# Kernel tuning notes

Measured on AMD Instinct MI355X. Metric: run time of the kernel, lower is better.

The kernel has to match this reference:

```python
import jax, jax.numpy as jnp
import numpy as np

NUM_CLASSES = 10
THRESHOLD = 2e-4
ENT_COEF = 2e-4
COS_EPS = 1e-8
LOG_EPS = 1e-12


def setup_inputs() -> dict:
    key = jax.random.key(0)
    k1, k2, k3 = jax.random.split(key, 3)
    B, C, H, W = 256, 256, 8, 8
    M, F = 2000, C * H * W
    z = jax.random.normal(k1, (B, C, H, W), dtype=jnp.float32)
    labels = jax.random.randint(k2, (B,), 0, NUM_CLASSES)
    # kaiming-uniform-like init for the memory table
    bound = float(np.sqrt(6.0 / F))
    memory = jax.random.uniform(k3, (M, F), dtype=jnp.float32, minval=-bound, maxval=bound)
    return {"z": z, "labels": labels, "memory": memory}


def _shrink_l1norm(w):
    # hardshrink (strict |x| > lambda) then L1 renormalize along memories
    w = jnp.where(jnp.abs(w) > THRESHOLD, w, jnp.zeros_like(w))
    return w / jnp.sum(jnp.abs(w), axis=1, keepdims=True)


def _entropy_loss(w):
    return ENT_COEF * jnp.sum(-w * jnp.log(w + LOG_EPS))


def reference(z, labels, memory):
    B, C, H, W = z.shape
    M, F = memory.shape
    zf = z.reshape(B, F)
    # cosine similarity without materializing (B, M, F): dot / max(||z||*||m||, eps)
    nz = jnp.linalg.norm(zf, axis=1)              # (B,)
    nm = jnp.linalg.norm(memory, axis=1)          # (M,)
    logit = (zf @ memory.T) / jnp.maximum(nz[:, None] * nm[None, :], COS_EPS)  # (B, M)
    mem_weight = jax.nn.softmax(logit, axis=1)
    # per-class masks: memory slots are partitioned contiguously per class
    mem_per_class = M // NUM_CLASSES
    cls_of_mem = jnp.arange(M) // mem_per_class   # (M,)
    m1 = (cls_of_mem[None, :] == labels[:, None]).astype(mem_weight.dtype)  # target mask
    m2 = 1.0 - m1
    w_t = _shrink_l1norm(mem_weight * m1)
    w_nt = _shrink_l1norm(mem_weight * m2)
    z_hat_target = (w_t @ memory).reshape(B, C, H, W)
    z_hat_non_target = (w_nt @ memory).reshape(B, C, H, W)
    return (z_hat_target, z_hat_non_target, _entropy_loss(w_t), _entropy_loss(w_nt))
```

## Files before the change

kernel.cpp:

```cpp
#include <hip/hip_runtime.h>
#include <math.h>

#define BATCH 256
#define FDIM 16384
#define MSLOTS 2000
#define MPAD 2048
#define NCLS 10
#define MPC 200
#define NFB (FDIM / 64)

static constexpr float THRESH = 2e-4f;
static constexpr float ENTC   = 2e-4f;
static constexpr float CEPS   = 1e-8f;
static constexpr float LEPS   = 1e-12f;

using bf16x8 = __attribute__((ext_vector_type(8))) short;
using f32x4  = __attribute__((ext_vector_type(4))) float;
using us8    = __attribute__((ext_vector_type(8))) unsigned short;

__device__ __forceinline__ unsigned short f2bf(float f) {
  unsigned u = __float_as_uint(f);
  unsigned r = u + 0x7fffu + ((u >> 16) & 1u);
  return (unsigned short)(r >> 16);
}
__device__ __forceinline__ float bf2f(unsigned short b) {
  return __uint_as_float(((unsigned)b) << 16);
}

__device__ __forceinline__ void gload_lds16(const unsigned short* g, unsigned short* l) {
  __builtin_amdgcn_global_load_lds(
      (const __attribute__((address_space(1))) void*)g,
      (__attribute__((address_space(3))) void*)l, 16, 0, 0);
}

__device__ __forceinline__ float waveReduceSum(float v) {
#pragma unroll
  for (int o = 32; o > 0; o >>= 1) v += __shfl_xor(v, o);
  return v;
}
__device__ __forceinline__ float waveReduceMax(float v) {
#pragma unroll
  for (int o = 32; o > 0; o >>= 1) v = fmaxf(v, __shfl_xor(v, o));
  return v;
}


__global__ __launch_bounds__(256) void convert_all_kernel(
    const float* __restrict__ z, const float* __restrict__ mem,
    unsigned short* __restrict__ zb, unsigned short* __restrict__ mb,
    unsigned short* __restrict__ mt, float* __restrict__ npart) {
  __shared__ unsigned int P[64 * 34];
  __shared__ float rsum[64][17];
  const int tid = threadIdx.x;
  const int f0 = blockIdx.x * 64;
  const int yt = blockIdx.y;
  const bool isMem = (yt < MPAD / 64);
  const int r0 = isMem ? yt * 64 : (yt - MPAD / 64) * 64;
  const float* src = isMem ? mem : z;
  unsigned short* dst = isMem ? mb : zb;

  const int q = tid & 15;
  const int mb0 = tid >> 4;

#pragma unroll
  for (int it = 0; it < 4; ++it) {
    const int m = mb0 + it * 16;
    const int gr = r0 + m;
    float4 v = make_float4(0.f, 0.f, 0.f, 0.f);
    if (!isMem || gr < MSLOTS)
      v = *reinterpret_cast<const float4*>(&src[(size_t)gr * FDIM + f0 + q * 4]);
    rsum[m][q] = fmaf(v.x, v.x, fmaf(v.y, v.y, fmaf(v.z, v.z, v.w * v.w)));
    unsigned lo = ((unsigned)f2bf(v.y) << 16) | f2bf(v.x);
    unsigned hi = ((unsigned)f2bf(v.w) << 16) | f2bf(v.z);
    *reinterpret_cast<uint2*>(&dst[(size_t)gr * FDIM + f0 + q * 4]) = make_uint2(lo, hi);
    if (isMem) {
      const int x = (m >> 1) & 15;
      const int col = 2 * (q ^ x);
      *reinterpret_cast<uint2*>(&P[m * 34 + col]) = make_uint2(lo, hi);
    }
  }
  __syncthreads();

  if (isMem) {
    const int h = tid & 7;
    const int j = tid >> 3;
    unsigned p[8];
#pragma unroll
    for (int s = 0; s < 8; ++s) {
      const int m = 8 * h + s;
      const int col = j ^ (((m >> 1) & 15) << 1);
      p[s] = P[m * 34 + col];
    }
    unsigned lo[4], hi[4];
#pragma unroll
    for (int t = 0; t < 4; ++t) {
      const unsigned p0 = p[2 * t], p1 = p[2 * t + 1];
      lo[t] = (p1 << 16) | (p0 & 0xFFFFu);
      hi[t] = (p1 & 0xFFFF0000u) | (p0 >> 16);
    }
    const size_t base0 = (size_t)(f0 + 2 * j) * MPAD + r0 + h * 8;
    *reinterpret_cast<uint4*>(&mt[base0])        = make_uint4(lo[0], lo[1], lo[2], lo[3]);
    *reinterpret_cast<uint4*>(&mt[base0 + MPAD]) = make_uint4(hi[0], hi[1], hi[2], hi[3]);
  }

  if (tid < 64) {
    float s = 0.f;
#pragma unroll
    for (int c = 0; c < 16; ++c) s += rsum[tid][c];
    const int row = isMem ? (r0 + tid) : (MPAD + r0 + tid);
    npart[(size_t)row * NFB + blockIdx.x] = s;
  }
}

__global__ __launch_bounds__(64) void normfin_kernel(const float* __restrict__ npart,
                                                     float* __restrict__ nm,
                                                     float* __restrict__ nz) {
  const int row = blockIdx.x;
  const int lane = threadIdx.x;
  const float* p = npart + (size_t)row * NFB;
  float s = 0.f;
#pragma unroll
  for (int k = 0; k < NFB / 64; ++k) s += p[lane + k * 64];
  s = waveReduceSum(s);
  if (lane == 0) {
    float v = sqrtf(s);
    if (row < MPAD) nm[row] = v;
    else            nz[row - MPAD] = v;
  }
}

#define G1_BM 128
#define G1_BN 64
#define G1_BK 64
#define SPLITK 8
#define KCHUNK (FDIM / SPLITK)

__global__ __launch_bounds__(256, 2) void gemm1_mfma(const unsigned short* __restrict__ zb,
                                                     const unsigned short* __restrict__ mb,
                                                     float* __restrict__ part) {
  __shared__ unsigned short As[G1_BM * G1_BK];
  __shared__ unsigned short Bs[G1_BN * G1_BK];
  const int tid = threadIdx.x;
  const int lane = tid & 63, wid = tid >> 6;
  const int bn0 = blockIdx.x * G1_BN;
  const int bm0 = blockIdx.y * G1_BM;
  const int kbase = blockIdx.z * KCHUNK;
  const int wr = wid >> 1, wc = wid & 1;
  const int l8 = lane >> 3, l7 = lane & 7;
  const int r16 = lane & 15, klane = lane >> 4;

  f32x4 acc[4][2] = {};

  for (int kt = 0; kt < KCHUNK; kt += G1_BK) {
    const int kg = kbase + kt;
#pragma unroll
    for (int it = 0; it < 4; ++it) {
      int c = wid + it * 4;
      int r = c * 8 + l8;
      int src = (l7 ^ (r & 7)) << 3;
      gload_lds16(&zb[(size_t)(bm0 + r) * FDIM + kg + src], &As[c * 512]);
    }
#pragma unroll
    for (int it = 0; it < 2; ++it) {
      int c = wid + it * 4;
      int r = c * 8 + l8;
      int src = (l7 ^ (r & 7)) << 3;
      gload_lds16(&mb[(size_t)(bn0 + r) * FDIM + kg + src], &Bs[c * 512]);
    }
    __syncthreads();
#pragma unroll
    for (int s = 0; s < 2; ++s) {
      bf16x8 a[4], bb[2];
#pragma unroll
      for (int i = 0; i < 4; ++i) {
        int r = wr * 64 + i * 16 + r16;
        int p = (s * 4 + klane) ^ (r & 7);
        a[i] = *reinterpret_cast<const bf16x8*>(&As[r * 64 + p * 8]);
      }
#pragma unroll
      for (int j = 0; j < 2; ++j) {
        int r = wc * 32 + j * 16 + r16;
        int p = (s * 4 + klane) ^ (r & 7);
        bb[j] = *reinterpret_cast<const bf16x8*>(&Bs[r * 64 + p * 8]);
      }
#pragma unroll
      for (int i = 0; i < 4; ++i)
#pragma unroll
        for (int j = 0; j < 2; ++j)
          acc[i][j] = __builtin_amdgcn_mfma_f32_16x16x32_bf16(a[i], bb[j], acc[i][j], 0, 0, 0);
    }
    __syncthreads();
  }
  const int rgrp = lane >> 4;
  float* pbase = part + (size_t)blockIdx.z * BATCH * MPAD;
#pragma unroll
  for (int i = 0; i < 4; ++i)
#pragma unroll
    for (int j = 0; j < 2; ++j)
#pragma unroll
      for (int rg = 0; rg < 4; ++rg) {
        int row = bm0 + wr * 64 + i * 16 + rgrp * 4 + rg;
        int col = bn0 + wc * 32 + j * 16 + r16;
        pbase[(size_t)row * MPAD + col] = acc[i][j][rg];
      }
}

__global__ __launch_bounds__(256) void softmax2_kernel(const float* __restrict__ part,
                                                       const float* __restrict__ nzv,
                                                       const float* __restrict__ nmv,
                                                       const int* __restrict__ labels,
                                                       unsigned short* __restrict__ wt,
                                                       unsigned short* __restrict__ wn,
                                                       float* __restrict__ ent) {
  const int b = blockIdx.x, tid = threadIdx.x;
  __shared__ float sh[MSLOTS];
  __shared__ float red[4], red2[4];
  const float nzb = nzv[b];
  float mx = -3.4e38f;
  for (int m = tid; m < MSLOTS; m += 256) {
    float s = 0.f;
#pragma unroll
    for (int sp = 0; sp < SPLITK; ++sp)
      s += part[((size_t)sp * BATCH + b) * MPAD + m];
    float v = s / fmaxf(nzb * nmv[m], CEPS);
    sh[m] = v; mx = fmaxf(mx, v);
  }
  mx = waveReduceMax(mx);
  if ((tid & 63) == 0) red[tid >> 6] = mx;
  __syncthreads();
  mx = fmaxf(fmaxf(red[0], red[1]), fmaxf(red[2], red[3]));
  __syncthreads();

  float s = 0.f;
  for (int m = tid; m < MSLOTS; m += 256) {
    float e = expf(sh[m] - mx); sh[m] = e; s += e;
  }
  s = waveReduceSum(s);
  if ((tid & 63) == 0) red[tid >> 6] = s;
  __syncthreads();
  s = red[0] + red[1] + red[2] + red[3];
  __syncthreads();

  const float inv = 1.f / s;
  const int c = labels[b];
  const int t0 = c * MPC, t1 = t0 + MPC;
  float st = 0.f, sn = 0.f;
  for (int m = tid; m < MSLOTS; m += 256) {
    float w = sh[m] * inv;
    float k = (w > THRESH) ? w : 0.f;
    sh[m] = k;
    bool tgt = (m >= t0) && (m < t1);
    st += tgt ? k : 0.f;
    sn += tgt ? 0.f : k;
  }
  st = waveReduceSum(st); sn = waveReduceSum(sn);
  if ((tid & 63) == 0) { red[tid >> 6] = st; red2[tid >> 6] = sn; }
  __syncthreads();
  st = red[0] + red[1] + red[2] + red[3];
  sn = red2[0] + red2[1] + red2[2] + red2[3];
  __syncthreads();

  const float rt = 1.f / st, rn = 1.f / sn;
  float et = 0.f, en = 0.f;
  unsigned short* wtr = wt + (size_t)b * MPAD;
  unsigned short* wnr = wn + (size_t)b * MPAD;
  for (int m = tid; m < MPAD; m += 256) {
    float a = 0.f, cn = 0.f;
    if (m < MSLOTS) {
      float k = sh[m];
      bool tgt = (m >= t0) && (m < t1);
      a  = tgt ? k * rt : 0.f;
      cn = tgt ? 0.f : k * rn;
      et -= a  * logf(a  + LEPS);
      en -= cn * logf(cn + LEPS);
    }
    wtr[m] = f2bf(a);
    wnr[m] = f2bf(cn);
  }
  et = waveReduceSum(et); en = waveReduceSum(en);
  if ((tid & 63) == 0) { red[tid >> 6] = et; red2[tid >> 6] = en; }
  __syncthreads();
  if (tid == 0) {
    ent[b]         = red[0] + red[1] + red[2] + red[3];
    ent[BATCH + b] = red2[0] + red2[1] + red2[2] + red2[3];
  }
}

#define G2_BM 128
#define G2_BN 128
#define G2_BK 64

__global__ __launch_bounds__(512, 2) void gemm23_mfma(const unsigned short* __restrict__ wt,
                                                      const unsigned short* __restrict__ wn,
                                                      const unsigned short* __restrict__ mt,
                                                      float* __restrict__ out) {
  __shared__ unsigned short At[G2_BM * G2_BK];
  __shared__ unsigned short An[G2_BM * G2_BK];
  __shared__ unsigned short Bs[G2_BN * G2_BK];
  const int tid = threadIdx.x, lane = tid & 63, wid = tid >> 6;
  const int bn0 = blockIdx.x * G2_BN;
  const int bm0 = blockIdx.y * G2_BM;
  const int wr = wid >> 2, wc = wid & 3;
  const int l8 = lane >> 3, l7 = lane & 7;
  const int r16 = lane & 15, klane = lane >> 4;

  f32x4 acct[4][2] = {}, accn[4][2] = {};

  for (int k0 = 0; k0 < MPAD; k0 += G2_BK) {
#pragma unroll
    for (int it = 0; it < 2; ++it) {
      int c = wid + it * 8;
      int r = c * 8 + l8;
      int src = (l7 ^ (r & 7)) << 3;
      gload_lds16(&wt[(size_t)(bm0 + r) * MPAD + k0 + src], &At[c * 512]);
      gload_lds16(&wn[(size_t)(bm0 + r) * MPAD + k0 + src], &An[c * 512]);
      gload_lds16(&mt[(size_t)(bn0 + r) * MPAD + k0 + src], &Bs[c * 512]);
    }
    __syncthreads();
#pragma unroll
    for (int s = 0; s < 2; ++s) {
      bf16x8 at[4], an[4], bb[2];
#pragma unroll
      for (int i = 0; i < 4; ++i) {
        int r = wr * 64 + i * 16 + r16;
        int p = (s * 4 + klane) ^ (r & 7);
        at[i] = *reinterpret_cast<const bf16x8*>(&At[r * 64 + p * 8]);
        an[i] = *reinterpret_cast<const bf16x8*>(&An[r * 64 + p * 8]);
      }
#pragma unroll
      for (int j = 0; j < 2; ++j) {
        int r = wc * 32 + j * 16 + r16;
        int p = (s * 4 + klane) ^ (r & 7);
        bb[j] = *reinterpret_cast<const bf16x8*>(&Bs[r * 64 + p * 8]);
      }
#pragma unroll
      for (int i = 0; i < 4; ++i)
#pragma unroll
        for (int j = 0; j < 2; ++j) {
          acct[i][j] = __builtin_amdgcn_mfma_f32_16x16x32_bf16(at[i], bb[j], acct[i][j], 0, 0, 0);
          accn[i][j] = __builtin_amdgcn_mfma_f32_16x16x32_bf16(an[i], bb[j], accn[i][j], 0, 0, 0);
        }
    }
    __syncthreads();
  }
  float* outn = out + (size_t)BATCH * FDIM;
  const int rgrp = lane >> 4;
#pragma unroll
  for (int i = 0; i < 4; ++i)
#pragma unroll
    for (int j = 0; j < 2; ++j)
#pragma unroll
      for (int rg = 0; rg < 4; ++rg) {
        size_t off = (size_t)(bm0 + wr * 64 + i * 16 + rgrp * 4 + rg) * FDIM
                   + bn0 + wc * 32 + j * 16 + r16;
        out[off]  = acct[i][j][rg];
        outn[off] = accn[i][j][rg];
      }
}

__global__ __launch_bounds__(256) void entreduce_kernel(const float* __restrict__ ent,
                                                        float* __restrict__ out) {
  const int tid = threadIdx.x;
  float v = ent[tid];
  float u = ent[BATCH + tid];
  v = waveReduceSum(v); u = waveReduceSum(u);
  __shared__ float r1[4], r2[4];
  if ((tid & 63) == 0) { r1[tid >> 6] = v; r2[tid >> 6] = u; }
  __syncthreads();
  if (tid == 0) {
    out[(size_t)2 * BATCH * FDIM]     = ENTC * (r1[0] + r1[1] + r1[2] + r1[3]);
    out[(size_t)2 * BATCH * FDIM + 1] = ENTC * (r2[0] + r2[1] + r2[2] + r2[3]);
  }
}

#define NM_OFF    0
#define NZ_OFF    2048
#define LOGIT_OFF 4096
#define WT_OFF    (LOGIT_OFF + 512000)
#define WNT_OFF   (WT_OFF + 512000)
#define ENT_OFF   (WNT_OFF + 512000)

__global__ __launch_bounds__(256) void rownorm_kernel(const float* __restrict__ x,
                                                      float* __restrict__ out, int cols) {
  const int r = blockIdx.x;
  const float4* xr = reinterpret_cast<const float4*>(x) + (size_t)r * (cols >> 2);
  const int n4 = cols >> 2;
  float s = 0.f;
  for (int i = threadIdx.x; i < n4; i += 256) {
    float4 v = xr[i];
    s = fmaf(v.x, v.x, s); s = fmaf(v.y, v.y, s);
    s = fmaf(v.z, v.z, s); s = fmaf(v.w, v.w, s);
  }
  s = waveReduceSum(s);
  __shared__ float red[4];
  if ((threadIdx.x & 63) == 0) red[threadIdx.x >> 6] = s;
  __syncthreads();
  if (threadIdx.x == 0) out[r] = sqrtf(red[0] + red[1] + red[2] + red[3]);
}

#define O1_BM 64
#define O1_BN 32
#define O1_BK 64
__global__ __launch_bounds__(256) void gemm1_kernel(const float* __restrict__ z,
                                                    const float* __restrict__ mem,
                                                    const float* __restrict__ nzv,
                                                    const float* __restrict__ nmv,
                                                    float* __restrict__ logit) {
  __shared__ float As[O1_BK][O1_BM];
  __shared__ float Bs[O1_BK][O1_BN];
  const int tid = threadIdx.x;
  const int bm0 = blockIdx.y * O1_BM;
  const int bn0 = blockIdx.x * O1_BN;
  const int tm = tid >> 4, tn = tid & 15;
  float acc[4][2] = {};
  for (int k0 = 0; k0 < FDIM; k0 += O1_BK) {
#pragma unroll
    for (int it = 0; it < 4; ++it) {
      int i = tid + it * 256;
      int row = i >> 4, c4 = i & 15;
      float4 v = *reinterpret_cast<const float4*>(&z[(size_t)(bm0 + row) * FDIM + k0 + c4 * 4]);
      As[c4 * 4 + 0][row] = v.x; As[c4 * 4 + 1][row] = v.y;
      As[c4 * 4 + 2][row] = v.z; As[c4 * 4 + 3][row] = v.w;
    }
#pragma unroll
    for (int it = 0; it < 2; ++it) {
      int i = tid + it * 256;
      int row = i >> 4, c4 = i & 15;
      int gm = bn0 + row;
      float4 v = make_float4(0.f, 0.f, 0.f, 0.f);
      if (gm < MSLOTS)
        v = *reinterpret_cast<const float4*>(&mem[(size_t)gm * FDIM + k0 + c4 * 4]);
      Bs[c4 * 4 + 0][row] = v.x; Bs[c4 * 4 + 1][row] = v.y;
      Bs[c4 * 4 + 2][row] = v.z; Bs[c4 * 4 + 3][row] = v.w;
    }
    __syncthreads();
#pragma unroll
    for (int kk = 0; kk < O1_BK; ++kk) {
      const float* ap = &As[kk][tm * 4];
      const float* bp = &Bs[kk][tn * 2];
      float a0 = ap[0], a1 = ap[1], a2 = ap[2], a3 = ap[3];
      float b0 = bp[0], b1 = bp[1];
      acc[0][0] = fmaf(a0, b0, acc[0][0]); acc[0][1] = fmaf(a0, b1, acc[0][1]);
      acc[1][0] = fmaf(a1, b0, acc[1][0]); acc[1][1] = fmaf(a1, b1, acc[1][1]);
      acc[2][0] = fmaf(a2, b0, acc[2][0]); acc[2][1] = fmaf(a2, b1, acc[2][1]);
      acc[3][0] = fmaf(a3, b0, acc[3][0]); acc[3][1] = fmaf(a3, b1, acc[3][1]);
    }
    __syncthreads();
  }
  float nzr[4];
#pragma unroll
  for (int i = 0; i < 4; ++i) nzr[i] = nzv[bm0 + tm * 4 + i];
#pragma unroll
  for (int j = 0; j < 2; ++j) {
    int col = bn0 + tn * 2 + j;
    if (col < MSLOTS) {
      float nmr = nmv[col];
#pragma unroll
      for (int i = 0; i < 4; ++i)
        logit[(size_t)(bm0 + tm * 4 + i) * MSLOTS + col] = acc[i][j] / fmaxf(nzr[i] * nmr, CEPS);
    }
  }
}

__global__ __launch_bounds__(256) void softmax_kernel(const float* __restrict__ logit,
                                                      const int* __restrict__ labels,
                                                      float* __restrict__ wt,
                                                      float* __restrict__ wnt,
                                                      float* __restrict__ ent) {
  const int b = blockIdx.x;
  const int tid = threadIdx.x;
  __shared__ float sh[MSLOTS];
  __shared__ float red[4], red2[4];
  const float* lrow = logit + (size_t)b * MSLOTS;
  float mx = -3.4e38f;
  for (int m = tid; m < MSLOTS; m += 256) {
    float v = lrow[m]; sh[m] = v; mx = fmaxf(mx, v);
  }
  mx = waveReduceMax(mx);
  if ((tid & 63) == 0) red[tid >> 6] = mx;
  __syncthreads();
  mx = fmaxf(fmaxf(red[0], red[1]), fmaxf(red[2], red[3]));
  __syncthreads();
  float s = 0.f;
  for (int m = tid; m < MSLOTS; m += 256) {
    float e = expf(sh[m] - mx); sh[m] = e; s += e;
  }
  s = waveReduceSum(s);
  if ((tid & 63) == 0) red[tid >> 6] = s;
  __syncthreads();
  s = red[0] + red[1] + red[2] + red[3];
  __syncthreads();
  const float inv = 1.f / s;
  const int c = labels[b];
  const int t0 = c * MPC, t1 = t0 + MPC;
  float st = 0.f, sn = 0.f;
  for (int m = tid; m < MSLOTS; m += 256) {
    float w = sh[m] * inv;
    float k = (w > THRESH) ? w : 0.f;
    sh[m] = k;
    bool tgt = (m >= t0) && (m < t1);
    st += tgt ? k : 0.f;
    sn += tgt ? 0.f : k;
  }
  st = waveReduceSum(st); sn = waveReduceSum(sn);
  if ((tid & 63) == 0) { red[tid >> 6] = st; red2[tid >> 6] = sn; }
  __syncthreads();
  st = red[0] + red[1] + red[2] + red[3];
  sn = red2[0] + red2[1] + red2[2] + red2[3];
  __syncthreads();
  const float rt = 1.f / st, rn = 1.f / sn;
  float et = 0.f, en = 0.f;
  float* wtr = wt + (size_t)b * MSLOTS;
  float* wnr = wnt + (size_t)b * MSLOTS;
  for (int m = tid; m < MSLOTS; m += 256) {
    float k = sh[m];
    bool tgt = (m >= t0) && (m < t1);
    float a  = tgt ? k * rt : 0.f;
    float cn = tgt ? 0.f : k * rn;
    wtr[m] = a;
    wnr[m] = cn;
    et -= a  * logf(a  + LEPS);
    en -= cn * logf(cn + LEPS);
  }
  et = waveReduceSum(et); en = waveReduceSum(en);
  if ((tid & 63) == 0) { red[tid >> 6] = et; red2[tid >> 6] = en; }
  __syncthreads();
  if (tid == 0) {
    ent[b]         = red[0] + red[1] + red[2] + red[3];
    ent[BATCH + b] = red2[0] + red2[1] + red2[2] + red2[3];
  }
}

#define O2_BM 64
#define O2_BN 64
#define O2_BK 32
__global__ __launch_bounds__(256) void gemm23_kernel(const float* __restrict__ wt,
                                                     const float* __restrict__ wnt,
                                                     const float* __restrict__ mem,
                                                     float* __restrict__ out) {
  __shared__ float Wts[O2_BK][O2_BM];
  __shared__ float Wns[O2_BK][O2_BM];
  __shared__ float Ms[O2_BK][O2_BN];
  const int tid = threadIdx.x;
  const int bm0 = blockIdx.y * O2_BM;
  const int bn0 = blockIdx.x * O2_BN;
  const int tm = tid >> 4, tn = tid & 15;
  float at[4][4] = {}, an[4][4] = {};
  for (int k0 = 0; k0 < MSLOTS; k0 += O2_BK) {
#pragma unroll
    for (int it = 0; it < 2; ++it) {
      int i = tid + it * 256;
      int row = i >> 3, c4 = i & 7;
      int gk = k0 + c4 * 4;
      float4 vt = make_float4(0.f, 0.f, 0.f, 0.f), vn = vt;
      if (gk < MSLOTS) {
        vt = *reinterpret_cast<const float4*>(&wt [(size_t)(bm0 + row) * MSLOTS + gk]);
        vn = *reinterpret_cast<const float4*>(&wnt[(size_t)(bm0 + row) * MSLOTS + gk]);
      }
      Wts[c4 * 4 + 0][row] = vt.x; Wts[c4 * 4 + 1][row] = vt.y;
      Wts[c4 * 4 + 2][row] = vt.z; Wts[c4 * 4 + 3][row] = vt.w;
      Wns[c4 * 4 + 0][row] = vn.x; Wns[c4 * 4 + 1][row] = vn.y;
      Wns[c4 * 4 + 2][row] = vn.z; Wns[c4 * 4 + 3][row] = vn.w;
    }
#pragma unroll
    for (int it = 0; it < 2; ++it) {
      int i = tid + it * 256;
      int row = i >> 4, c4 = i & 15;
      int gk = k0 + row;
      float4 v = make_float4(0.f, 0.f, 0.f, 0.f);
      if (gk < MSLOTS)
        v = *reinterpret_cast<const float4*>(&mem[(size_t)gk * FDIM + bn0 + c4 * 4]);
      *reinterpret_cast<float4*>(&Ms[row][c4 * 4]) = v;
    }
    __syncthreads();
#pragma unroll
    for (int kk = 0; kk < O2_BK; ++kk) {
      const float* tp = &Wts[kk][tm * 4];
      const float* np = &Wns[kk][tm * 4];
      const float* bp = &Ms[kk][tn * 4];
      float b0 = bp[0], b1 = bp[1], b2 = bp[2], b3 = bp[3];
#pragma unroll
      for (int i = 0; i < 4; ++i) {
        float a = tp[i], cn = np[i];
        at[i][0] = fmaf(a,  b0, at[i][0]); at[i][1] = fmaf(a,  b1, at[i][1]);
        at[i][2] = fmaf(a,  b2, at[i][2]); at[i][3] = fmaf(a,  b3, at[i][3]);
        an[i][0] = fmaf(cn, b0, an[i][0]); an[i][1] = fmaf(cn, b1, an[i][1]);
        an[i][2] = fmaf(cn, b2, an[i][2]); an[i][3] = fmaf(cn, b3, an[i][3]);
      }
    }
    __syncthreads();
  }
  float* outt = out;
  float* outn = out + (size_t)BATCH * FDIM;
#pragma unroll
  for (int i = 0; i < 4; ++i) {
    size_t off = (size_t)(bm0 + tm * 4 + i) * FDIM + bn0 + tn * 4;
    *reinterpret_cast<float4*>(&outt[off]) = make_float4(at[i][0], at[i][1], at[i][2], at[i][3]);
    *reinterpret_cast<float4*>(&outn[off]) = make_float4(an[i][0], an[i][1], an[i][2], an[i][3]);
  }
}

extern "C" void kernel_launch(void* const* d_in, const int* in_sizes, int n_in,
                              void* d_out, int out_size, void* d_ws, size_t ws_size,
                              hipStream_t stream) {
  const float* z      = (const float*)d_in[0];
  const int*   labels = (const int*)d_in[1];
  const float* mem    = (const float*)d_in[2];
  float* out = (float*)d_out;
  char*  wsb = (char*)d_ws;

  constexpr size_t NM_B   = 0;
  constexpr size_t NZ_B   = 8192;
  constexpr size_t ZB_B   = 16384;
  constexpr size_t MB_B   = ZB_B + (size_t)BATCH * FDIM * 2;
  constexpr size_t MT_B   = MB_B + (size_t)MPAD * FDIM * 2;
  constexpr size_t WTB_B  = MT_B + (size_t)FDIM * MPAD * 2;
  constexpr size_t WNB_B  = WTB_B + (size_t)BATCH * MPAD * 2;
  constexpr size_t NP_B   = WNB_B + (size_t)BATCH * MPAD * 2;
  constexpr size_t PART_B = NP_B + (size_t)(MPAD + BATCH) * NFB * 4;
  constexpr size_t ENT_B  = PART_B + (size_t)SPLITK * BATCH * MPAD * 4;
  constexpr size_t NEED   = ENT_B + 2048;

  if (ws_size >= NEED) {
    float* nm = (float*)(wsb + NM_B);
    float* nz = (float*)(wsb + NZ_B);
    unsigned short* zb = (unsigned short*)(wsb + ZB_B);
    unsigned short* mb = (unsigned short*)(wsb + MB_B);
    unsigned short* mt = (unsigned short*)(wsb + MT_B);
    unsigned short* wt = (unsigned short*)(wsb + WTB_B);
    unsigned short* wn = (unsigned short*)(wsb + WNB_B);
    float* npart = (float*)(wsb + NP_B);
    float* part  = (float*)(wsb + PART_B);
    float* ent   = (float*)(wsb + ENT_B);

    convert_all_kernel<<<dim3(NFB, (MPAD + BATCH) / 64), 256, 0, stream>>>(
        z, mem, zb, mb, mt, npart);
    normfin_kernel<<<MPAD + BATCH, 64, 0, stream>>>(npart, nm, nz);
    gemm1_mfma<<<dim3(MPAD / G1_BN, BATCH / G1_BM, SPLITK), 256, 0, stream>>>(zb, mb, part);
    softmax2_kernel<<<BATCH, 256, 0, stream>>>(part, nz, nm, labels, wt, wn, ent);
    gemm23_mfma<<<dim3(FDIM / G2_BN, BATCH / G2_BM), 512, 0, stream>>>(wt, wn, mt, out);
    entreduce_kernel<<<1, 256, 0, stream>>>(ent, out);
  } else {
    float* ws    = (float*)d_ws;
    float* nm    = ws + NM_OFF;
    float* nzv   = ws + NZ_OFF;
    float* logit = ws + LOGIT_OFF;
    float* wt    = ws + WT_OFF;
    float* wnt   = ws + WNT_OFF;
    float* ent   = ws + ENT_OFF;

    rownorm_kernel<<<MSLOTS, 256, 0, stream>>>(mem, nm, FDIM);
    rownorm_kernel<<<BATCH, 256, 0, stream>>>(z, nzv, FDIM);
    gemm1_kernel<<<dim3((MSLOTS + O1_BN - 1) / O1_BN, BATCH / O1_BM), 256, 0, stream>>>(
        z, mem, nzv, nm, logit);
    softmax_kernel<<<BATCH, 256, 0, stream>>>(logit, labels, wt, wnt, ent);
    gemm23_kernel<<<dim3(FDIM / O2_BN, BATCH / O2_BM), 256, 0, stream>>>(wt, wnt, mem, out);
    entreduce_kernel<<<1, 256, 0, stream>>>(ent, out);
  }
}
```

Measured before the change: 150.9 us.

## Split conversion into row-streaming convert with fused norms and separate transpose

Replaces the tiled convert kernel, which wrote partial norms, plus the norm-finish kernel, with a per-row streaming kernel. It converts fp32 to bf16 and computes each row's norm in one block, then runs a separate transpose kernel that reads the bf16 memory to build the transposed copy. This removes the partial-norm buffer and one launch, and gives fully contiguous row reads and writes. In exchange it adds an extra read of the bf16 memory table for the transpose. Padded rows are zero-filled with a norm of 1.

```diff
diff --git a/kernel.cpp b/kernel.cpp
--- a/kernel.cpp
+++ b/kernel.cpp
@@ -7,7 +7,6 @@
 #define MPAD 2048
 #define NCLS 10
 #define MPC 200
-#define NFB (FDIM / 64)
 
 static constexpr float THRESH = 2e-4f;
 static constexpr float ENTC   = 2e-4f;
@@ -23,9 +22,6 @@
   unsigned r = u + 0x7fffu + ((u >> 16) & 1u);
   return (unsigned short)(r >> 16);
 }
-__device__ __forceinline__ float bf2f(unsigned short b) {
-  return __uint_as_float(((unsigned)b) << 16);
-}
 
 __device__ __forceinline__ void gload_lds16(const unsigned short* g, unsigned short* l) {
   __builtin_amdgcn_global_load_lds(
@@ -45,50 +41,76 @@
 }
 
 
-__global__ __launch_bounds__(256) void convert_all_kernel(
+__global__ __launch_bounds__(256) void convert_stream_kernel(
     const float* __restrict__ z, const float* __restrict__ mem,
     unsigned short* __restrict__ zb, unsigned short* __restrict__ mb,
-    unsigned short* __restrict__ mt, float* __restrict__ npart) {
-  __shared__ unsigned int P[64 * 34];
-  __shared__ float rsum[64][17];
+    float* __restrict__ nm, float* __restrict__ nz) {
+  const int row = blockIdx.x;
+  const bool isMem = (row < MPAD);
   const int tid = threadIdx.x;
-  const int f0 = blockIdx.x * 64;
-  const int yt = blockIdx.y;
-  const bool isMem = (yt < MPAD / 64);
-  const int r0 = isMem ? yt * 64 : (yt - MPAD / 64) * 64;
-  const float* src = isMem ? mem : z;
-  unsigned short* dst = isMem ? mb : zb;
-
-  const int q = tid & 15;
-  const int mb0 = tid >> 4;
-
+  unsigned short* orow = isMem ? (mb + (size_t)row * FDIM)
+                               : (zb + (size_t)(row - MPAD) * FDIM);
+  if (isMem && row >= MSLOTS) {
+    const uint4 zed = make_uint4(0u, 0u, 0u, 0u);
+    for (int i = tid; i < FDIM / 8; i += 256)
+      *reinterpret_cast<uint4*>(&orow[i * 8]) = zed;
+    if (tid == 0) nm[row] = 1.0f;
+    return;
+  }
+  const float* srow = isMem ? (mem + (size_t)row * FDIM)
+                            : (z + (size_t)(row - MPAD) * FDIM);
+  float s = 0.f;
+  for (int i = tid; i < FDIM / 8; i += 256) {
+    float4 a = *reinterpret_cast<const float4*>(&srow[i * 8]);
+    float4 b = *reinterpret_cast<const float4*>(&srow[i * 8 + 4]);
+    s = fmaf(a.x, a.x, fmaf(a.y, a.y, fmaf(a.z, a.z, fmaf(a.w, a.w, s))));
+    s = fmaf(b.x, b.x, fmaf(b.y, b.y, fmaf(b.z, b.z, fmaf(b.w, b.w, s))));
+    uint4 o;
+    o.x = ((unsigned)f2bf(a.y) << 16) | f2bf(a.x);
+    o.y = ((unsigned)f2bf(a.w) << 16) | f2bf(a.z);
+    o.z = ((unsigned)f2bf(b.y) << 16) | f2bf(b.x);
+    o.w = ((unsigned)f2bf(b.w) << 16) | f2bf(b.z);
+    *reinterpret_cast<uint4*>(&orow[i * 8]) = o;
+  }
+  s = waveReduceSum(s);
+  __shared__ float red[4];
+  if ((tid & 63) == 0) red[tid >> 6] = s;
+  __syncthreads();
+  if (tid == 0) {
+    float v = sqrtf(red[0] + red[1] + red[2] + red[3]);
+    if (isMem) nm[row] = v;
+    else       nz[row - MPAD] = v;
+  }
+}
+
+#define TR_M 128
+#define TR_F 64
+__global__ __launch_bounds__(256) void transpose_kernel(const unsigned short* __restrict__ mb,
+                                                        unsigned short* __restrict__ mt) {
+  __shared__ unsigned int P[TR_M * 34];
+  const int tid = threadIdx.x;
+  const int f0 = blockIdx.x * TR_F;
+  const int m0 = blockIdx.y * TR_M;
 #pragma unroll
   for (int it = 0; it < 4; ++it) {
-    const int m = mb0 + it * 16;
-    const int gr = r0 + m;
-    float4 v = make_float4(0.f, 0.f, 0.f, 0.f);
-    if (!isMem || gr < MSLOTS)
-      v = *reinterpret_cast<const float4*>(&src[(size_t)gr * FDIM + f0 + q * 4]);
-    rsum[m][q] = fmaf(v.x, v.x, fmaf(v.y, v.y, fmaf(v.z, v.z, v.w * v.w)));
-    unsigned lo = ((unsigned)f2bf(v.y) << 16) | f2bf(v.x);
-    unsigned hi = ((unsigned)f2bf(v.w) << 16) | f2bf(v.z);
-    *reinterpret_cast<uint2*>(&dst[(size_t)gr * FDIM + f0 + q * 4]) = make_uint2(lo, hi);
-    if (isMem) {
-      const int x = (m >> 1) & 15;
-      const int col = 2 * (q ^ x);
-      *reinterpret_cast<uint2*>(&P[m * 34 + col]) = make_uint2(lo, hi);
-    }
-  }
-  __syncthreads();
-
-  if (isMem) {
-    const int h = tid & 7;
-    const int j = tid >> 3;
+    const int r = (tid >> 3) + it * 32;
+    const int c8 = tid & 7;
+    const uint4 v = *reinterpret_cast<const uint4*>(
+        &mb[(size_t)(m0 + r) * FDIM + f0 + c8 * 8]);
+    const int x = (r >> 1) & 15;
+    *reinterpret_cast<uint2*>(&P[r * 34 + 2 * ((2 * c8) ^ x)])     = make_uint2(v.x, v.y);
+    *reinterpret_cast<uint2*>(&P[r * 34 + 2 * ((2 * c8 + 1) ^ x)]) = make_uint2(v.z, v.w);
+  }
+  __syncthreads();
+#pragma unroll
+  for (int half = 0; half < 2; ++half) {
+    const int h = tid & 15;
+    const int fp = (tid >> 4) + half * 16;
     unsigned p[8];
 #pragma unroll
     for (int s = 0; s < 8; ++s) {
-      const int m = 8 * h + s;
-      const int col = j ^ (((m >> 1) & 15) << 1);
+      const int m = h * 8 + s;
+      const int col = fp ^ ((((m >> 1) & 15)) << 1);
       p[s] = P[m * 34 + col];
     }
     unsigned lo[4], hi[4];
@@ -98,34 +120,9 @@
       lo[t] = (p1 << 16) | (p0 & 0xFFFFu);
       hi[t] = (p1 & 0xFFFF0000u) | (p0 >> 16);
     }
-    const size_t base0 = (size_t)(f0 + 2 * j) * MPAD + r0 + h * 8;
-    *reinterpret_cast<uint4*>(&mt[base0])        = make_uint4(lo[0], lo[1], lo[2], lo[3]);
-    *reinterpret_cast<uint4*>(&mt[base0 + MPAD]) = make_uint4(hi[0], hi[1], hi[2], hi[3]);
-  }
-
-  if (tid < 64) {
-    float s = 0.f;
-#pragma unroll
-    for (int c = 0; c < 16; ++c) s += rsum[tid][c];
-    const int row = isMem ? (r0 + tid) : (MPAD + r0 + tid);
-    npart[(size_t)row * NFB + blockIdx.x] = s;
-  }
-}
-
-__global__ __launch_bounds__(64) void normfin_kernel(const float* __restrict__ npart,
-                                                     float* __restrict__ nm,
-                                                     float* __restrict__ nz) {
-  const int row = blockIdx.x;
-  const int lane = threadIdx.x;
-  const float* p = npart + (size_t)row * NFB;
-  float s = 0.f;
-#pragma unroll
-  for (int k = 0; k < NFB / 64; ++k) s += p[lane + k * 64];
-  s = waveReduceSum(s);
-  if (lane == 0) {
-    float v = sqrtf(s);
-    if (row < MPAD) nm[row] = v;
-    else            nz[row - MPAD] = v;
+    const size_t base = (size_t)(f0 + 2 * fp) * MPAD + m0 + h * 8;
+    *reinterpret_cast<uint4*>(&mt[base])        = make_uint4(lo[0], lo[1], lo[2], lo[3]);
+    *reinterpret_cast<uint4*>(&mt[base + MPAD]) = make_uint4(hi[0], hi[1], hi[2], hi[3]);
   }
 }
 
@@ -616,8 +613,7 @@
   constexpr size_t MT_B   = MB_B + (size_t)MPAD * FDIM * 2;
   constexpr size_t WTB_B  = MT_B + (size_t)FDIM * MPAD * 2;
   constexpr size_t WNB_B  = WTB_B + (size_t)BATCH * MPAD * 2;
-  constexpr size_t NP_B   = WNB_B + (size_t)BATCH * MPAD * 2;
-  constexpr size_t PART_B = NP_B + (size_t)(MPAD + BATCH) * NFB * 4;
+  constexpr size_t PART_B = WNB_B + (size_t)BATCH * MPAD * 2;
   constexpr size_t ENT_B  = PART_B + (size_t)SPLITK * BATCH * MPAD * 4;
   constexpr size_t NEED   = ENT_B + 2048;
 
@@ -629,13 +625,11 @@
     unsigned short* mt = (unsigned short*)(wsb + MT_B);
     unsigned short* wt = (unsigned short*)(wsb + WTB_B);
     unsigned short* wn = (unsigned short*)(wsb + WNB_B);
-    float* npart = (float*)(wsb + NP_B);
     float* part  = (float*)(wsb + PART_B);
     float* ent   = (float*)(wsb + ENT_B);
 
-    convert_all_kernel<<<dim3(NFB, (MPAD + BATCH) / 64), 256, 0, stream>>>(
-        z, mem, zb, mb, mt, npart);
-    normfin_kernel<<<MPAD + BATCH, 64, 0, stream>>>(npart, nm, nz);
+    convert_stream_kernel<<<MPAD + BATCH, 256, 0, stream>>>(z, mem, zb, mb, nm, nz);
+    transpose_kernel<<<dim3(FDIM / TR_F, MPAD / TR_M), 256, 0, stream>>>(mb, mt);
     gemm1_mfma<<<dim3(MPAD / G1_BN, BATCH / G1_BM, SPLITK), 256, 0, stream>>>(zb, mb, part);
     softmax2_kernel<<<BATCH, 256, 0, stream>>>(part, nz, nm, labels, wt, wn, ent);
     gemm23_mfma<<<dim3(FDIM / G2_BN, BATCH / G2_BM), 512, 0, stream>>>(wt, wn, mt, out);
```

After: 157.5 us. +4.4%, slower.

## Stage fp32 tiles via global_load_lds and widen convert tile to 128 columns

Applied to the files above, without the earlier changes.

The conversion kernel now loads each 64x128 fp32 tile straight into LDS with async global_load_lds, then reads it from shared memory for the bf16 conversion, norm partials and transpose, instead of doing per-thread float4 global loads. The tile width doubles to 128 features, which halves the grid and the number of norm partials per row, and the norm finalize step shrinks to two loads per lane. The aim is better memory-level parallelism on this bandwidth-bound preprocessing pass. The cost is more LDS per block (about 57KB), which may lower occupancy, and out-of-range memory rows are clamped on load and then masked.

```diff
diff --git a/kernel.cpp b/kernel.cpp
--- a/kernel.cpp
+++ b/kernel.cpp
@@ -7,7 +7,7 @@
 #define MPAD 2048
 #define NCLS 10
 #define MPC 200
-#define NFB (FDIM / 64)
+#define NFB2 128
 
 static constexpr float THRESH = 2e-4f;
 static constexpr float ENTC   = 2e-4f;
@@ -23,15 +23,17 @@
   unsigned r = u + 0x7fffu + ((u >> 16) & 1u);
   return (unsigned short)(r >> 16);
 }
-__device__ __forceinline__ float bf2f(unsigned short b) {
-  return __uint_as_float(((unsigned)b) << 16);
-}
 
 __device__ __forceinline__ void gload_lds16(const unsigned short* g, unsigned short* l) {
   __builtin_amdgcn_global_load_lds(
       (const __attribute__((address_space(1))) void*)g,
       (__attribute__((address_space(3))) void*)l, 16, 0, 0);
 }
+__device__ __forceinline__ void gload_lds16f(const float* g, float* l) {
+  __builtin_amdgcn_global_load_lds(
+      (const __attribute__((address_space(1))) void*)g,
+      (__attribute__((address_space(3))) void*)l, 16, 0, 0);
+}
 
 __device__ __forceinline__ float waveReduceSum(float v) {
 #pragma unroll
@@ -49,66 +51,79 @@
     const float* __restrict__ z, const float* __restrict__ mem,
     unsigned short* __restrict__ zb, unsigned short* __restrict__ mb,
     unsigned short* __restrict__ mt, float* __restrict__ npart) {
-  __shared__ unsigned int P[64 * 34];
-  __shared__ float rsum[64][17];
+  __shared__ float F[64 * 128];
+  __shared__ unsigned int P[64 * 66];
+  __shared__ float rsum[64 * 33];
   const int tid = threadIdx.x;
-  const int f0 = blockIdx.x * 64;
+  const int lane = tid & 63, wid = tid >> 6;
+  const int f0 = blockIdx.x * 128;
   const int yt = blockIdx.y;
   const bool isMem = (yt < MPAD / 64);
   const int r0 = isMem ? yt * 64 : (yt - MPAD / 64) * 64;
   const float* src = isMem ? mem : z;
   unsigned short* dst = isMem ? mb : zb;
 
-  const int q = tid & 15;
-  const int mb0 = tid >> 4;
-
-#pragma unroll
-  for (int it = 0; it < 4; ++it) {
-    const int m = mb0 + it * 16;
+#pragma unroll
+  for (int it = 0; it < 8; ++it) {
+    const int c = wid * 8 + it;
+    int gr = r0 + 2 * c + (lane >> 5);
+    if (isMem && gr >= MSLOTS) gr = MSLOTS - 1;
+    gload_lds16f(&src[(size_t)gr * FDIM + f0 + (lane & 31) * 4], &F[c * 256]);
+  }
+  __syncthreads();
+
+  const int q = tid & 31;
+  const int mb8 = tid >> 5;
+  const int fq = f0 + q * 4;
+#pragma unroll
+  for (int it = 0; it < 8; ++it) {
+    const int m = mb8 + it * 8;
     const int gr = r0 + m;
+    const bool valid = !isMem || gr < MSLOTS;
     float4 v = make_float4(0.f, 0.f, 0.f, 0.f);
-    if (!isMem || gr < MSLOTS)
-      v = *reinterpret_cast<const float4*>(&src[(size_t)gr * FDIM + f0 + q * 4]);
-    rsum[m][q] = fmaf(v.x, v.x, fmaf(v.y, v.y, fmaf(v.z, v.z, v.w * v.w)));
+    if (valid) v = *reinterpret_cast<const float4*>(&F[m * 128 + q * 4]);
+    rsum[m * 33 + q] = fmaf(v.x, v.x, fmaf(v.y, v.y, fmaf(v.z, v.z, v.w * v.w)));
     unsigned lo = ((unsigned)f2bf(v.y) << 16) | f2bf(v.x);
     unsigned hi = ((unsigned)f2bf(v.w) << 16) | f2bf(v.z);
-    *reinterpret_cast<uint2*>(&dst[(size_t)gr * FDIM + f0 + q * 4]) = make_uint2(lo, hi);
+    *reinterpret_cast<uint2*>(&dst[(size_t)gr * FDIM + fq]) = make_uint2(lo, hi);
     if (isMem) {
       const int x = (m >> 1) & 15;
-      const int col = 2 * (q ^ x);
-      *reinterpret_cast<uint2*>(&P[m * 34 + col]) = make_uint2(lo, hi);
+      *reinterpret_cast<uint2*>(&P[m * 66 + 2 * (q ^ x)]) = make_uint2(lo, hi);
     }
   }
   __syncthreads();
 
   if (isMem) {
     const int h = tid & 7;
-    const int j = tid >> 3;
-    unsigned p[8];
-#pragma unroll
-    for (int s = 0; s < 8; ++s) {
-      const int m = 8 * h + s;
-      const int col = j ^ (((m >> 1) & 15) << 1);
-      p[s] = P[m * 34 + col];
-    }
-    unsigned lo[4], hi[4];
-#pragma unroll
-    for (int t = 0; t < 4; ++t) {
-      const unsigned p0 = p[2 * t], p1 = p[2 * t + 1];
-      lo[t] = (p1 << 16) | (p0 & 0xFFFFu);
-      hi[t] = (p1 & 0xFFFF0000u) | (p0 >> 16);
-    }
-    const size_t base0 = (size_t)(f0 + 2 * j) * MPAD + r0 + h * 8;
-    *reinterpret_cast<uint4*>(&mt[base0])        = make_uint4(lo[0], lo[1], lo[2], lo[3]);
-    *reinterpret_cast<uint4*>(&mt[base0 + MPAD]) = make_uint4(hi[0], hi[1], hi[2], hi[3]);
-  }
-
+    const int j0 = tid >> 3;
+#pragma unroll
+    for (int half = 0; half < 2; ++half) {
+      const int j = j0 + half * 32;
+      unsigned p[8];
+#pragma unroll
+      for (int s = 0; s < 8; ++s) {
+        const int m = h * 8 + s;
+        const int col = j ^ (((m >> 1) & 15) << 1);
+        p[s] = P[m * 66 + col];
+      }
+      unsigned lo[4], hi[4];
+#pragma unroll
+      for (int t = 0; t < 4; ++t) {
+        const unsigned p0 = p[2 * t], p1 = p[2 * t + 1];
+        lo[t] = (p1 << 16) | (p0 & 0xFFFFu);
+        hi[t] = (p1 & 0xFFFF0000u) | (p0 >> 16);
+      }
+      const size_t base = (size_t)(f0 + 2 * j) * MPAD + r0 + h * 8;
+      *reinterpret_cast<uint4*>(&mt[base])        = make_uint4(lo[0], lo[1], lo[2], lo[3]);
+      *reinterpret_cast<uint4*>(&mt[base + MPAD]) = make_uint4(hi[0], hi[1], hi[2], hi[3]);
+    }
+  }
   if (tid < 64) {
     float s = 0.f;
 #pragma unroll
-    for (int c = 0; c < 16; ++c) s += rsum[tid][c];
+    for (int c = 0; c < 32; ++c) s += rsum[tid * 33 + c];
     const int row = isMem ? (r0 + tid) : (MPAD + r0 + tid);
-    npart[(size_t)row * NFB + blockIdx.x] = s;
+    npart[(size_t)row * NFB2 + blockIdx.x] = s;
   }
 }
 
@@ -117,10 +132,8 @@
                                                      float* __restrict__ nz) {
   const int row = blockIdx.x;
   const int lane = threadIdx.x;
-  const float* p = npart + (size_t)row * NFB;
-  float s = 0.f;
-#pragma unroll
-  for (int k = 0; k < NFB / 64; ++k) s += p[lane + k * 64];
+  const float* p = npart + (size_t)row * NFB2;
+  float s = p[lane] + p[lane + 64];
   s = waveReduceSum(s);
   if (lane == 0) {
     float v = sqrtf(s);
@@ -617,7 +630,7 @@
   constexpr size_t WTB_B  = MT_B + (size_t)FDIM * MPAD * 2;
   constexpr size_t WNB_B  = WTB_B + (size_t)BATCH * MPAD * 2;
   constexpr size_t NP_B   = WNB_B + (size_t)BATCH * MPAD * 2;
-  constexpr size_t PART_B = NP_B + (size_t)(MPAD + BATCH) * NFB * 4;
+  constexpr size_t PART_B = NP_B + (size_t)(MPAD + BATCH) * NFB2 * 4;
   constexpr size_t ENT_B  = PART_B + (size_t)SPLITK * BATCH * MPAD * 4;
   constexpr size_t NEED   = ENT_B + 2048;
 
@@ -633,7 +646,7 @@
     float* part  = (float*)(wsb + PART_B);
     float* ent   = (float*)(wsb + ENT_B);
 
-    convert_all_kernel<<<dim3(NFB, (MPAD + BATCH) / 64), 256, 0, stream>>>(
+    convert_all_kernel<<<dim3(FDIM / 128, (MPAD + BATCH) / 64), 256, 0, stream>>>(
         z, mem, zb, mb, mt, npart);
     normfin_kernel<<<MPAD + BATCH, 64, 0, stream>>>(npart, nm, nz);
     gemm1_mfma<<<dim3(MPAD / G1_BN, BATCH / G1_BM, SPLITK), 256, 0, stream>>>(zb, mb, part);
```

After: 146.9 us (median of 2 runs). -2.7%, faster.
